# Kernel tuning notes

Hardware: AMD Instinct MI355X
Metric: run time of the kernel (lower is better)

Reference implementation:

```python
import jax, jax.numpy as jnp
import numpy as np
from jax import lax


def setup_inputs() -> dict:
    key = jax.random.key(0)
    k1, k2 = jax.random.split(key)
    B, Cin, T, H, W_ = 4, 16, 31, 128, 128
    Chid = 16
    inputs = jax.random.normal(k1, (B, Cin, T, H, W_), dtype=jnp.float32)
    # Conv3d(Cin, 2*Chid, kernel=3, padding=1) weights, OIDHW layout
    W = jax.random.normal(k2, (2 * Chid, Cin, 3, 3, 3), dtype=jnp.float32) * 0.05
    b = jnp.zeros((2 * Chid,), dtype=jnp.float32)
    return {"inputs": inputs, "W": W, "b": b}


def _fo_pool(Z, F):
    # Z, F: [B, C, T, H, W]; recurrence h_t = f_t * h_{t-1} + (1 - f_t) * z_t, h_{-1} = 0
    Zt = jnp.moveaxis(Z, 2, 0)  # [T, B, C, H, W]
    Ft = jnp.moveaxis(F, 2, 0)

    def step(h, zf):
        z, f = zf
        h = f * h + (1.0 - f) * z
        return h, h

    h0 = jnp.zeros_like(Zt[0])
    _, hs = lax.scan(step, h0, (Zt, Ft))
    return jnp.moveaxis(hs, 0, 2)  # back to [B, C, T, H, W]


def reference(inputs, W, b):
    # gated conv: Conv3d with SAME padding (kernel 3, padding 1)
    gates = lax.conv_general_dilated(
        inputs, W, window_strides=(1, 1, 1), padding="SAME",
        dimension_numbers=("NCDHW", "OIDHW", "NCDHW"))
    gates = gates + b[None, :, None, None, None]
    Chid = W.shape[0] // 2
    Z = jnp.tanh(gates[:, :Chid])
    F = jax.nn.sigmoid(gates[:, Chid:])
    return _fo_pool(Z, F)
```

## Files before the change

kernel.cpp:

```cpp
#include <hip/hip_runtime.h>
#include <cstdint>
#include <cstddef>

#define CIN     16
#define CHID    16
#define T_DIM   31
#define HW_     16384
#define CH_STRIDE 507904
#define TILE_H  8
#define TILE_W  32
#define SH      10
#define SW      34
#define SPOS    (SH * SW)
#define PSTR    24
#define SLICE_SH (SPOS * PSTR)
#define NSLOT   4

typedef short bf16x8 __attribute__((ext_vector_type(8)));
typedef float f32x16 __attribute__((ext_vector_type(16)));

__device__ __forceinline__ unsigned bf16_bits(float x) {
  unsigned u = __builtin_bit_cast(unsigned, x);
  u += 0x7FFFu + ((u >> 16) & 1u);
  return u >> 16;
}
__device__ __forceinline__ unsigned cvt_pk_bf16(float lo, float hi) {
  unsigned r;
  asm("v_cvt_pk_bf16_f32 %0, %1, %2" : "=v"(r) : "v"(lo), "v"(hi));
  return r;
}

__global__ __launch_bounds__(512, 2)
void qrnn3d_v15(const float* __restrict__ in, const float* __restrict__ Wg,
                const float* __restrict__ bg, float* __restrict__ out) {
  __shared__ __align__(16) short xs[NSLOT][SLICE_SH];

  const int tid = threadIdx.x;
  const int bid = blockIdx.x;
  const int lin  = ((bid & 7) << 5) | (bid >> 3);
  const int b    = lin >> 6;
  const int tile = lin & 63;
  const int h0   = (tile >> 2) * TILE_H;
  const int w0   = (tile & 3) * TILE_W;

  const int lane = tid & 63;
  const int wid  = tid >> 6;
  const int col  = lane & 31;
  const int half = lane >> 5;

  bf16x8 wfrag[27];
#pragma unroll
  for (int tau = 0; tau < 27; ++tau) {
    bf16x8 f;
#pragma unroll
    for (int j = 0; j < 8; ++j)
      f[j] = (short)bf16_bits(Wg[col * 432 + (half * 8 + j) * 27 + tau]);
    wfrag[tau] = f;
  }

  f32x16 accInit;
  int voff[8];
#pragma unroll
  for (int r = 0; r < 8; ++r) {
    int oc = (r & 3) + 8 * (r >> 2) + 4 * half;
    accInit[r]     = bg[oc];
    accInit[r + 8] = bg[oc + 16];
    voff[r] = (b * CHID + oc) * CH_STRIDE + (h0 + wid) * 128 + (w0 + col);
  }

  const float* gp[3];
  int  lso[3];
  bool stv[3], ldv[3];
#pragma unroll
  for (int i = 0; i < 3; ++i) {
    int p   = tid + i * 512;
    int q   = p & 15;
    int c4  = (p >> 4) & 3;
    int j   = p >> 6;
    int pos = j * 16 + q;
    stv[i]  = (pos < SPOS);
    int hh  = pos / SW;
    int ww  = pos - hh * SW;
    int gh  = h0 + hh - 1, gw = w0 + ww - 1;
    ldv[i]  = stv[i] && ((unsigned)gh < 128u) && ((unsigned)gw < 128u);
    int sp  = ldv[i] ? (gh * 128 + gw) : 0;
    gp[i]   = in + (size_t)(b * CIN + c4 * 4) * CH_STRIDE + sp;
    lso[i]  = pos * PSTR + c4 * 4;
  }

#define LOADV(tz, vv)                                                \
  do {                                                               \
    if ((tz) <= 30) {                                                \
      const int toff = (tz) * HW_;                                   \
      _Pragma("unroll")                                              \
      for (int i = 0; i < 3; ++i) {                                  \
        _Pragma("unroll")                                            \
        for (int k = 0; k < 4; ++k)                                  \
          vv[i][k] = ldv[i] ? gp[i][toff + k * CH_STRIDE] : 0.0f;    \
      }                                                              \
    } else {                                                         \
      _Pragma("unroll")                                              \
      for (int i = 0; i < 3; ++i) {                                  \
        _Pragma("unroll")                                            \
        for (int k = 0; k < 4; ++k) vv[i][k] = 0.0f;                 \
      }                                                              \
    }                                                                \
  } while (0)

#define STOREV(vv, slot)                                             \
  do {                                                               \
    short* dst = &xs[(slot)][0];                                     \
    _Pragma("unroll")                                                \
    for (int i = 0; i < 3; ++i) {                                    \
      if (stv[i]) {                                                  \
        uint2 u;                                                     \
        u.x = cvt_pk_bf16(vv[i][0], vv[i][1]);                       \
        u.y = cvt_pk_bf16(vv[i][2], vv[i][3]);                       \
        *reinterpret_cast<uint2*>(dst + lso[i]) = u;                 \
      }                                                              \
    }                                                                \
  } while (0)

  int lb[9];
#pragma unroll
  for (int kh = 0; kh < 3; ++kh)
#pragma unroll
    for (int kw = 0; kw < 3; ++kw)
      lb[kh * 3 + kw] = ((wid + kh) * SW + (col + kw)) * PSTR + half * 8;

  float hst[8];
#pragma unroll
  for (int r = 0; r < 8; ++r) hst[r] = 0.0f;

  const float C_TANH = 2.8853900817779268f;
  const float C_SIG  = 1.4426950408889634f;

  auto compute = [&](int t) {
    const short* base = &xs[0][0];
    const short* sA = base + ((t + 3) & 3) * SLICE_SH;
    const short* sB = base + ((t    ) & 3) * SLICE_SH;
    const short* sC = base + ((t + 1) & 3) * SLICE_SH;

    f32x16 acc0 = accInit;
    f32x16 acc1;
#pragma unroll
    for (int i = 0; i < 16; ++i) acc1[i] = 0.0f;

#pragma unroll
    for (int kd = 0; kd < 3; ++kd) {
      const short* sp = (kd == 0) ? sA : (kd == 1) ? sB : sC;
#pragma unroll
      for (int u = 0; u < 9; ++u) {
        const int tau = kd * 9 + u;
        bf16x8 xb = *reinterpret_cast<const bf16x8*>(sp + lb[u]);
        if (tau & 1)
          acc1 = __builtin_amdgcn_mfma_f32_32x32x16_bf16(wfrag[tau], xb, acc1, 0, 0, 0);
        else
          acc0 = __builtin_amdgcn_mfma_f32_32x32x16_bf16(wfrag[tau], xb, acc0, 0, 0, 0);
      }
    }

    float* outT = out + (size_t)t * HW_;
#pragma unroll
    for (int r = 0; r < 8; ++r) {
      float zg = acc0[r] + acc1[r];
      float fg = acc0[r + 8] + acc1[r + 8];
      float ez = exp2f(zg * C_TANH);
      float z  = __builtin_fmaf(-2.0f, __builtin_amdgcn_rcpf(ez + 1.0f), 1.0f);
      float ef = exp2f(-fg * C_SIG);
      float f  = __builtin_amdgcn_rcpf(1.0f + ef);
      float h  = __builtin_fmaf(f, hst[r] - z, z);
      hst[r]   = h;
      outT[voff[r]] = h;
    }
  };

  float vA[3][4], vB[3][4];
  LOADV(0, vA); STOREV(vA, 0);
  LOADV(1, vA); STOREV(vA, 1);
  LOADV(2, vA);
  for (int i = tid; i < SLICE_SH / 2; i += 512)
    reinterpret_cast<unsigned*>(&xs[3][0])[i] = 0u;
  __syncthreads();

#pragma unroll 1
  for (int t = 0; t < 30; t += 2) {
    LOADV(t + 3, vB);
    STOREV(vA, (t + 2) & 3);
    compute(t);
    __syncthreads();
    LOADV(t + 4, vA);
    STOREV(vB, (t + 3) & 3);
    compute(t + 1);
    __syncthreads();
  }
  compute(30);

#undef LOADV
#undef STOREV
}

extern "C" void kernel_launch(void* const* d_in, const int* in_sizes, int n_in,
                              void* d_out, int out_size, void* d_ws, size_t ws_size,
                              hipStream_t stream) {
  const float* in = (const float*)d_in[0];
  const float* Wg = (const float*)d_in[1];
  const float* bg = (const float*)d_in[2];
  float* out      = (float*)d_out;
  (void)in_sizes; (void)n_in; (void)out_size; (void)d_ws; (void)ws_size;
  qrnn3d_v15<<<dim3(256), dim3(512), 0, stream>>>(in, Wg, bg, out);
}
```

Measured before the change: 119.2 us.

## Deepen LDS ring to six slots and sync once per two timesteps

Grows the shared-memory slice ring from four to six slots, held in dynamic shared memory, so two future time slices can be staged while two timesteps are computed. Each loop iteration now stores two prefetched slices, issues global loads for the next two, runs two conv+recurrence steps, and ends with a single barrier, halving the barriers. The aim is to cut synchronization stalls and hide global load latency behind more compute. In exchange it uses more LDS per block and keeps more prefetch values live in registers.

```diff
diff --git a/kernel.cpp b/kernel.cpp
--- a/kernel.cpp
+++ b/kernel.cpp
@@ -14,7 +14,7 @@
 #define SPOS    (SH * SW)
 #define PSTR    24
 #define SLICE_SH (SPOS * PSTR)
-#define NSLOT   4
+#define NSLOT   6
 
 typedef short bf16x8 __attribute__((ext_vector_type(8)));
 typedef float f32x16 __attribute__((ext_vector_type(16)));
@@ -31,9 +31,9 @@
 }
 
 __global__ __launch_bounds__(512, 2)
-void qrnn3d_v15(const float* __restrict__ in, const float* __restrict__ Wg,
+void qrnn3d_v16(const float* __restrict__ in, const float* __restrict__ Wg,
                 const float* __restrict__ bg, float* __restrict__ out) {
-  __shared__ __align__(16) short xs[NSLOT][SLICE_SH];
+  extern __shared__ __align__(16) short xs[];
 
   const int tid = threadIdx.x;
   const int bid = blockIdx.x;
@@ -109,7 +109,7 @@
 
 #define STOREV(vv, slot)                                             \
   do {                                                               \
-    short* dst = &xs[(slot)][0];                                     \
+    short* dst = xs + (slot) * SLICE_SH;                             \
     _Pragma("unroll")                                                \
     for (int i = 0; i < 3; ++i) {                                    \
       if (stv[i]) {                                                  \
@@ -135,11 +135,10 @@
   const float C_TANH = 2.8853900817779268f;
   const float C_SIG  = 1.4426950408889634f;
 
-  auto compute = [&](int t) {
-    const short* base = &xs[0][0];
-    const short* sA = base + ((t + 3) & 3) * SLICE_SH;
-    const short* sB = base + ((t    ) & 3) * SLICE_SH;
-    const short* sC = base + ((t + 1) & 3) * SLICE_SH;
+  auto compute = [&](int t, int sa, int sb, int sc) {
+    const short* sA = xs + sa * SLICE_SH;
+    const short* sB = xs + sb * SLICE_SH;
+    const short* sC = xs + sc * SLICE_SH;
 
     f32x16 acc0 = accInit;
     f32x16 acc1;
@@ -178,23 +177,30 @@
   float vA[3][4], vB[3][4];
   LOADV(0, vA); STOREV(vA, 0);
   LOADV(1, vA); STOREV(vA, 1);
-  LOADV(2, vA);
+  LOADV(2, vA); STOREV(vA, 2);
   for (int i = tid; i < SLICE_SH / 2; i += 512)
-    reinterpret_cast<unsigned*>(&xs[3][0])[i] = 0u;
+    reinterpret_cast<unsigned*>(xs + 5 * SLICE_SH)[i] = 0u;
+  LOADV(3, vA);
+  LOADV(4, vB);
   __syncthreads();
 
 #pragma unroll 1
-  for (int t = 0; t < 30; t += 2) {
-    LOADV(t + 3, vB);
-    STOREV(vA, (t + 2) & 3);
-    compute(t);
+  for (int ts = 0; ts < 30; ts += 2) {
+    const int m0 = ts % 6;
+    const int m1 = (ts + 1) % 6;
+    const int m2 = (ts + 2) % 6;
+    const int m3 = (ts + 3) % 6;
+    const int m4 = (ts + 4) % 6;
+    const int m5 = (ts + 5) % 6;
+    STOREV(vA, m3);
+    STOREV(vB, m4);
+    LOADV(ts + 5, vA);
+    LOADV(ts + 6, vB);
+    compute(ts,     m5, m0, m1);
+    compute(ts + 1, m0, m1, m2);
     __syncthreads();
-    LOADV(t + 4, vA);
-    STOREV(vB, (t + 3) & 3);
-    compute(t + 1);
-    __syncthreads();
-  }
-  compute(30);
+  }
+  compute(30, 5, 0, 1);
 
 #undef LOADV
 #undef STOREV
@@ -208,5 +214,5 @@
   const float* bg = (const float*)d_in[2];
   float* out      = (float*)d_out;
   (void)in_sizes; (void)n_in; (void)out_size; (void)d_ws; (void)ws_size;
-  qrnn3d_v15<<<dim3(256), dim3(512), 0, stream>>>(in, Wg, bg, out);
-}
+  qrnn3d_v16<<<dim3(256), dim3(512), NSLOT * SLICE_SH * sizeof(short), stream>>>(in, Wg, bg, out);
+}
```

Result: slower. 306.5 us (+157.1%).
